# Kernel optimization log

Measured on AMD Instinct MI355X. Metric: run time of the kernel, lower is better.

## Reference

```python
import jax, jax.numpy as jnp
import numpy as np

OUT_F, IN_F = 4096, 4096
GROUP = 128
NGROUPS = IN_F // GROUP  # 32


def setup_inputs() -> dict:
    key = jax.random.key(0)
    k1, k2, k3, k4 = jax.random.split(key, 4)
    x = jax.random.normal(k1, (4, 2048, IN_F), dtype=jnp.float32)
    # 4-bit codes stored as integers in [0, 16)
    compressed_weight = jax.random.randint(k2, (OUT_F, IN_F), 0, 16, dtype=jnp.int32)
    scale = jax.random.uniform(k3, (OUT_F, NGROUPS), dtype=jnp.float32)
    offset = jax.random.normal(k4, (OUT_F, NGROUPS), dtype=jnp.float32)
    return {"x": x, "compressed_weight": compressed_weight, "scale": scale, "offset": offset}


def reference(x, compressed_weight, scale, offset):
    # group-wise dequant: w[o, g, j] = code * scale[o, g] - offset[o, g]
    codes = compressed_weight.astype(scale.dtype).reshape(OUT_F, NGROUPS, GROUP)
    w = (codes * scale[..., None] - offset[..., None]).reshape(OUT_F, IN_F)
    # F.linear: x @ w.T  -> [B, S, OUT_F]
    return jnp.einsum('bsi,oi->bso', x, w.astype(x.dtype))
```

## Files before the change

kernel.cpp:

```cpp
#include <hip/hip_runtime.h>
#include <stdint.h>

#define OUT_F 4096
#define IN_F  4096
#define NGROUPS 32
#define BK 64
#define NT (IN_F / BK)

typedef __attribute__((ext_vector_type(4))) float    f32x4;
typedef __attribute__((ext_vector_type(8))) short    bf16x8;
typedef __attribute__((ext_vector_type(4))) int      i32x4;
typedef __attribute__((ext_vector_type(4))) uint32_t u32x4;

__device__ __forceinline__ ushort f2bf(float f) {
  union { float f; uint32_t u; } v; v.f = f;
  uint32_t r = v.u + 0x7FFFu + ((v.u >> 16) & 1u);
  return (ushort)(r >> 16);
}

__global__ void cvt_x_kernel(const float* __restrict__ x, ushort* __restrict__ xb, int n8) {
  int i = blockIdx.x * blockDim.x + threadIdx.x;
  if (i >= n8) return;
  const f32x4* xp = (const f32x4*)x;
  f32x4 a = xp[2 * i], b = xp[2 * i + 1];
  u32x4 o;
  o.x = (uint32_t)f2bf(a.x) | ((uint32_t)f2bf(a.y) << 16);
  o.y = (uint32_t)f2bf(a.z) | ((uint32_t)f2bf(a.w) << 16);
  o.z = (uint32_t)f2bf(b.x) | ((uint32_t)f2bf(b.y) << 16);
  o.w = (uint32_t)f2bf(b.z) | ((uint32_t)f2bf(b.w) << 16);
  ((u32x4*)xb)[i] = o;
}

__global__ void dequant_w_kernel(const int* __restrict__ cw,
                                 const float* __restrict__ sc,
                                 const float* __restrict__ of,
                                 ushort* __restrict__ wb) {
  int t = blockIdx.x * blockDim.x + threadIdx.x;
  int o  = t >> 9;
  int k0 = (t & 511) << 3;
  int g  = k0 >> 7;
  float s   = sc[o * NGROUPS + g];
  float off = of[o * NGROUPS + g];
  const i32x4* cp = (const i32x4*)(cw + (size_t)o * IN_F + k0);
  i32x4 c0 = cp[0], c1 = cp[1];
  u32x4 out;
  out.x = (uint32_t)f2bf((float)c0.x * s - off) | ((uint32_t)f2bf((float)c0.y * s - off) << 16);
  out.y = (uint32_t)f2bf((float)c0.z * s - off) | ((uint32_t)f2bf((float)c0.w * s - off) << 16);
  out.z = (uint32_t)f2bf((float)c1.x * s - off) | ((uint32_t)f2bf((float)c1.y * s - off) << 16);
  out.w = (uint32_t)f2bf((float)c1.z * s - off) | ((uint32_t)f2bf((float)c1.w * s - off) << 16);
  *(u32x4*)(wb + (size_t)o * IN_F + k0) = out;
}


#define BAR() do { asm volatile("" ::: "memory"); __builtin_amdgcn_s_barrier(); asm volatile("" ::: "memory"); } while (0)

#define GLLDS(gp, lp) __builtin_amdgcn_global_load_lds( \
  (const __attribute__((address_space(1))) uint32_t*)(const void*)(gp), \
  (__attribute__((address_space(3))) uint32_t*)(void*)(lp), 16, 0, 0)

#define STAGE_A(buf, kt) do { \
  _Pragma("unroll") for (int h_ = 0; h_ < 2; ++h_) \
  _Pragma("unroll") for (int c_ = 0; c_ < 2; ++c_) \
    GLLDS(A + (size_t)(m0 + h_ * 128 + c_ * 64 + stRow) * IN_F + (kt) * BK + sl * 8, \
          ldsb + (buf) * 65536 + h_ * 16384 + c_ * 8192 + wid * 1024); \
} while (0)

#define STAGE_B_HALF(buf, kt, h_) do { \
  _Pragma("unroll") for (int c_ = 0; c_ < 2; ++c_) \
    GLLDS(B + (size_t)(n0 + (h_) * 128 + c_ * 64 + stRow) * IN_F + (kt) * BK + sl * 8, \
          ldsb + (buf) * 65536 + 32768 + (h_) * 16384 + c_ * 8192 + wid * 1024); \
} while (0)

#define RD_A(base, i0) do { \
  _Pragma("unroll") for (int i_ = 0; i_ < 4; ++i_) { \
    Ar[i_][0] = *(const bf16x8*)((base) + ((i0) + i_) * 2048 + off0); \
    Ar[i_][1] = *(const bf16x8*)((base) + ((i0) + i_) * 2048 + off1); \
  } } while (0)

#define RD_B(dst, j0) do { \
  _Pragma("unroll") for (int j_ = 0; j_ < 2; ++j_) { \
    dst[j_][0] = *(const bf16x8*)(bC + ((j0) + j_) * 2048 + off0); \
    dst[j_][1] = *(const bf16x8*)(bC + ((j0) + j_) * 2048 + off1); \
  } } while (0)

#define MFMAQ(I0, J0, Bset) do { \
  __builtin_amdgcn_s_setprio(1); \
  _Pragma("unroll") for (int i_ = 0; i_ < 4; ++i_) \
  _Pragma("unroll") for (int j_ = 0; j_ < 2; ++j_) { \
    acc[(I0) + i_][(J0) + j_] = __builtin_amdgcn_mfma_f32_16x16x32_bf16(Ar[i_][0], Bset[j_][0], acc[(I0) + i_][(J0) + j_], 0, 0, 0); \
    acc[(I0) + i_][(J0) + j_] = __builtin_amdgcn_mfma_f32_16x16x32_bf16(Ar[i_][1], Bset[j_][1], acc[(I0) + i_][(J0) + j_], 0, 0, 0); \
  } \
  __builtin_amdgcn_s_setprio(0); \
} while (0)

__global__ __launch_bounds__(512, 2) void gemm256(const ushort* __restrict__ A,
                                                  const ushort* __restrict__ B,
                                                  float* __restrict__ C, int M) {
  __shared__ ushort lds[65536];
  char* ldsb = (char*)lds;

  const int nmt = M >> 8;
  const int nwg = gridDim.x;
  int wg = blockIdx.x;
  if ((nwg & 7) == 0) wg = (wg & 7) * (nwg >> 3) + (wg >> 3);
  const int bn = wg / nmt;
  const int bm = wg % nmt;
  const int m0 = bm << 8, n0 = bn << 8;

  const int tid  = threadIdx.x;
  const int lane = tid & 63;
  const int wid  = tid >> 6;
  const int wr   = wid >> 2;
  const int wc   = wid & 3;

  const int stRow = wid * 8 + (lane >> 3);
  const int sl    = (lane & 7) ^ (lane >> 3);

  const int frow = lane & 15;
  const int g    = lane >> 4;
  const int off0 = frow * 128 + (((g    ) ^ (lane & 7)) << 4);
  const int off1 = frow * 128 + (((4 + g) ^ (lane & 7)) << 4);

  f32x4 acc[8][4] = {};
  bf16x8 Ar[4][2], Bl[2][2], Bh[2][2];

  STAGE_A(0, 0);
  STAGE_B_HALF(0, 0, 0);
  STAGE_B_HALF(0, 0, 1);
  STAGE_A(1, 1);
  asm volatile("s_waitcnt vmcnt(4)" ::: "memory");
  BAR();
  RD_A(ldsb + wr * 16384, 0);

#pragma unroll 1
  for (int t = 0; t < NT; ++t) {
    const int cur = t & 1, nxt = cur ^ 1;
    const char* aC = ldsb + cur * 65536 + wr * 16384;
    const char* aN = ldsb + nxt * 65536 + wr * 16384;
    const char* bC = ldsb + cur * 65536 + 32768 + (wc >> 1) * 16384 + (wc & 1) * 8192;

    RD_B(Bl, 0);
    RD_B(Bh, 2);
    if (t + 1 < NT) STAGE_B_HALF(nxt, t + 1, 0);
    BAR();
    MFMAQ(0, 0, Bl);

    if (t + 1 < NT) STAGE_B_HALF(nxt, t + 1, 1);
    BAR();
    MFMAQ(0, 2, Bh);
    RD_A(aC, 4);
    if (t + 1 < NT) { asm volatile("s_waitcnt vmcnt(4)" ::: "memory"); }
    BAR();

    MFMAQ(4, 2, Bh);
    BAR();

    if (t + 2 < NT) STAGE_A(cur, t + 2);
    MFMAQ(4, 0, Bl);
    if (t + 1 < NT) {
      RD_A(aN, 0);
      if (t + 2 < NT) { asm volatile("s_waitcnt vmcnt(4)" ::: "memory"); }
      else            { asm volatile("s_waitcnt vmcnt(0)" ::: "memory"); }
    }
    BAR();
  }

  const int crow0 = m0 + wr * 128 + (g << 2);
  const int ccol0 = n0 + wc * 64 + frow;
#pragma unroll
  for (int mf = 0; mf < 8; ++mf)
#pragma unroll
    for (int nf = 0; nf < 4; ++nf)
#pragma unroll
      for (int q = 0; q < 4; ++q)
        C[(size_t)(crow0 + mf * 16 + q) * OUT_F + (ccol0 + nf * 16)] = acc[mf][nf][q];
}

__global__ void naive_kernel(const float* __restrict__ x, const int* __restrict__ cw,
                             const float* __restrict__ sc, const float* __restrict__ of,
                             float* __restrict__ out, int M) {
  int idx = blockIdx.x * blockDim.x + threadIdx.x;
  if (idx >= M * OUT_F) return;
  int o = idx & (OUT_F - 1);
  int m = idx >> 12;
  const float* xr = x + (size_t)m * IN_F;
  const int*   wr = cw + (size_t)o * IN_F;
  float acc = 0.f;
  for (int gg = 0; gg < NGROUPS; ++gg) {
    float s = sc[o * NGROUPS + gg], off = of[o * NGROUPS + gg];
#pragma unroll 8
    for (int k = 0; k < 128; ++k) {
      int kk = (gg << 7) + k;
      acc += xr[kk] * ((float)wr[kk] * s - off);
    }
  }
  out[idx] = acc;
}

extern "C" void kernel_launch(void* const* d_in, const int* in_sizes, int n_in,
                              void* d_out, int out_size, void* d_ws, size_t ws_size,
                              hipStream_t stream) {
  const float* x  = (const float*)d_in[0];
  const int*   cw = (const int*)d_in[1];
  const float* sc = (const float*)d_in[2];
  const float* of = (const float*)d_in[3];
  float* out = (float*)d_out;
  const int M = in_sizes[0] / IN_F;

  const size_t xb_bytes = (size_t)M * IN_F * 2;
  const size_t wb_bytes = (size_t)OUT_F * IN_F * 2;

  if (ws_size >= xb_bytes + wb_bytes && (M % 256) == 0) {
    ushort* xb = (ushort*)d_ws;
    ushort* wb = (ushort*)((char*)d_ws + xb_bytes);

    int n8 = (M * IN_F) / 8;
    cvt_x_kernel<<<(n8 + 255) / 256, 256, 0, stream>>>(x, xb, n8);

    int nw8 = (OUT_F * IN_F) / 8;
    dequant_w_kernel<<<(nw8 + 255) / 256, 256, 0, stream>>>(cw, sc, of, wb);

    dim3 grid((M / 256) * (OUT_F / 256));
    gemm256<<<grid, 512, 0, stream>>>(xb, wb, out, M);
  } else {
    int total = M * OUT_F;
    naive_kernel<<<(total + 255) / 256, 256, 0, stream>>>(x, cw, sc, of, out, M);
  }
}
```

Baseline: 291.0 us.

## Switch GEMM to 32x32x16 MFMA with k-sliced double-buffered register pipeline

Replaces the 16x16x32 bf16 MFMA tiling with 32x32x16 MFMA instructions, so each wave computes 4x2 32x32 tiles per k-slice. The main loop is restructured to ping-pong register fragment sets across four k-slices, with A and B staged together for tile t+2 and one fewer barrier per iteration. The aim is fewer LDS reads per FLOP and better MFMA issue density. In exchange the vmcnt bookkeeping and epilogue store layout change, and the bigger accumulator fragments may raise register pressure.

```diff
diff --git a/kernel.cpp b/kernel.cpp
--- a/kernel.cpp
+++ b/kernel.cpp
@@ -7,10 +7,11 @@
 #define BK 64
 #define NT (IN_F / BK)
 
-typedef __attribute__((ext_vector_type(4))) float    f32x4;
-typedef __attribute__((ext_vector_type(8))) short    bf16x8;
-typedef __attribute__((ext_vector_type(4))) int      i32x4;
-typedef __attribute__((ext_vector_type(4))) uint32_t u32x4;
+typedef __attribute__((ext_vector_type(4)))  float    f32x4;
+typedef __attribute__((ext_vector_type(16))) float    f32x16;
+typedef __attribute__((ext_vector_type(8)))  short    bf16x8;
+typedef __attribute__((ext_vector_type(4)))  int      i32x4;
+typedef __attribute__((ext_vector_type(4)))  uint32_t u32x4;
 
 __device__ __forceinline__ ushort f2bf(float f) {
   union { float f; uint32_t u; } v; v.f = f;
@@ -59,37 +60,29 @@
   (__attribute__((address_space(3))) uint32_t*)(void*)(lp), 16, 0, 0)
 
 #define STAGE_A(buf, kt) do { \
-  _Pragma("unroll") for (int h_ = 0; h_ < 2; ++h_) \
-  _Pragma("unroll") for (int c_ = 0; c_ < 2; ++c_) \
-    GLLDS(A + (size_t)(m0 + h_ * 128 + c_ * 64 + stRow) * IN_F + (kt) * BK + sl * 8, \
-          ldsb + (buf) * 65536 + h_ * 16384 + c_ * 8192 + wid * 1024); \
-} while (0)
-
-#define STAGE_B_HALF(buf, kt, h_) do { \
-  _Pragma("unroll") for (int c_ = 0; c_ < 2; ++c_) \
-    GLLDS(B + (size_t)(n0 + (h_) * 128 + c_ * 64 + stRow) * IN_F + (kt) * BK + sl * 8, \
-          ldsb + (buf) * 65536 + 32768 + (h_) * 16384 + c_ * 8192 + wid * 1024); \
-} while (0)
-
-#define RD_A(base, i0) do { \
-  _Pragma("unroll") for (int i_ = 0; i_ < 4; ++i_) { \
-    Ar[i_][0] = *(const bf16x8*)((base) + ((i0) + i_) * 2048 + off0); \
-    Ar[i_][1] = *(const bf16x8*)((base) + ((i0) + i_) * 2048 + off1); \
-  } } while (0)
-
-#define RD_B(dst, j0) do { \
-  _Pragma("unroll") for (int j_ = 0; j_ < 2; ++j_) { \
-    dst[j_][0] = *(const bf16x8*)(bC + ((j0) + j_) * 2048 + off0); \
-    dst[j_][1] = *(const bf16x8*)(bC + ((j0) + j_) * 2048 + off1); \
-  } } while (0)
-
-#define MFMAQ(I0, J0, Bset) do { \
+  _Pragma("unroll") for (int q_ = 0; q_ < 4; ++q_) \
+    GLLDS(A + (size_t)(m0 + q_ * 64 + stRow) * IN_F + (kt) * BK + sl * 8, \
+          ldsb + (buf) * 65536 + q_ * 8192 + wid * 1024); \
+} while (0)
+
+#define STAGE_B(buf, kt) do { \
+  _Pragma("unroll") for (int q_ = 0; q_ < 4; ++q_) \
+    GLLDS(B + (size_t)(n0 + q_ * 64 + stRow) * IN_F + (kt) * BK + sl * 8, \
+          ldsb + (buf) * 65536 + 32768 + q_ * 8192 + wid * 1024); \
+} while (0)
+
+#define RD_SLICE(SET, S, aX, bX) do { \
+  _Pragma("unroll") for (int i_ = 0; i_ < 4; ++i_) \
+    A_[SET][i_] = *(const bf16x8*)((aX) + (i_ * 32 + lw) * 128 + kOff[S]); \
+  _Pragma("unroll") for (int j_ = 0; j_ < 2; ++j_) \
+    B_[SET][j_] = *(const bf16x8*)((bX) + (j_ * 32 + lw) * 128 + kOff[S]); \
+} while (0)
+
+#define MFMA_SLICE(SET) do { \
   __builtin_amdgcn_s_setprio(1); \
   _Pragma("unroll") for (int i_ = 0; i_ < 4; ++i_) \
-  _Pragma("unroll") for (int j_ = 0; j_ < 2; ++j_) { \
-    acc[(I0) + i_][(J0) + j_] = __builtin_amdgcn_mfma_f32_16x16x32_bf16(Ar[i_][0], Bset[j_][0], acc[(I0) + i_][(J0) + j_], 0, 0, 0); \
-    acc[(I0) + i_][(J0) + j_] = __builtin_amdgcn_mfma_f32_16x16x32_bf16(Ar[i_][1], Bset[j_][1], acc[(I0) + i_][(J0) + j_], 0, 0, 0); \
-  } \
+  _Pragma("unroll") for (int j_ = 0; j_ < 2; ++j_) \
+    acc[i_][j_] = __builtin_amdgcn_mfma_f32_32x32x16_bf16(A_[SET][i_], B_[SET][j_], acc[i_][j_], 0, 0, 0); \
   __builtin_amdgcn_s_setprio(0); \
 } while (0)
 
@@ -116,64 +109,56 @@
   const int stRow = wid * 8 + (lane >> 3);
   const int sl    = (lane & 7) ^ (lane >> 3);
 
-  const int frow = lane & 15;
-  const int g    = lane >> 4;
-  const int off0 = frow * 128 + (((g    ) ^ (lane & 7)) << 4);
-  const int off1 = frow * 128 + (((4 + g) ^ (lane & 7)) << 4);
-
-  f32x4 acc[8][4] = {};
-  bf16x8 Ar[4][2], Bl[2][2], Bh[2][2];
-
-  STAGE_A(0, 0);
-  STAGE_B_HALF(0, 0, 0);
-  STAGE_B_HALF(0, 0, 1);
-  STAGE_A(1, 1);
-  asm volatile("s_waitcnt vmcnt(4)" ::: "memory");
+  const int lw = lane & 31;
+  const int h  = lane >> 5;
+  int kOff[4];
+#pragma unroll
+  for (int s = 0; s < 4; ++s) kOff[s] = ((2 * s + h) ^ (lane & 7)) << 4;
+
+  f32x16 acc[4][2] = {};
+  bf16x8 A_[2][4], B_[2][2];
+
+  STAGE_A(0, 0); STAGE_B(0, 0);
+  STAGE_A(1, 1); STAGE_B(1, 1);
+  asm volatile("s_waitcnt vmcnt(8)" ::: "memory");
   BAR();
-  RD_A(ldsb + wr * 16384, 0);
+  RD_SLICE(0, 0, ldsb + wr * 16384, ldsb + 32768 + wc * 8192);
 
 #pragma unroll 1
   for (int t = 0; t < NT; ++t) {
     const int cur = t & 1, nxt = cur ^ 1;
     const char* aC = ldsb + cur * 65536 + wr * 16384;
+    const char* bC = ldsb + cur * 65536 + 32768 + wc * 8192;
     const char* aN = ldsb + nxt * 65536 + wr * 16384;
-    const char* bC = ldsb + cur * 65536 + 32768 + (wc >> 1) * 16384 + (wc & 1) * 8192;
-
-    RD_B(Bl, 0);
-    RD_B(Bh, 2);
-    if (t + 1 < NT) STAGE_B_HALF(nxt, t + 1, 0);
+    const char* bN = ldsb + nxt * 65536 + 32768 + wc * 8192;
+
+    RD_SLICE(1, 1, aC, bC);
+    MFMA_SLICE(0);
+    RD_SLICE(0, 2, aC, bC);
+    MFMA_SLICE(1);
     BAR();
-    MFMAQ(0, 0, Bl);
-
-    if (t + 1 < NT) STAGE_B_HALF(nxt, t + 1, 1);
+
+    RD_SLICE(1, 3, aC, bC);
+    if (t + 2 < NT) { STAGE_A(cur, t + 2); STAGE_B(cur, t + 2); }
+    MFMA_SLICE(0);
+    if (t + 2 < NT)      { asm volatile("s_waitcnt vmcnt(8)" ::: "memory"); }
+    else if (t + 1 < NT) { asm volatile("s_waitcnt vmcnt(0)" ::: "memory"); }
     BAR();
-    MFMAQ(0, 2, Bh);
-    RD_A(aC, 4);
-    if (t + 1 < NT) { asm volatile("s_waitcnt vmcnt(4)" ::: "memory"); }
-    BAR();
-
-    MFMAQ(4, 2, Bh);
-    BAR();
-
-    if (t + 2 < NT) STAGE_A(cur, t + 2);
-    MFMAQ(4, 0, Bl);
-    if (t + 1 < NT) {
-      RD_A(aN, 0);
-      if (t + 2 < NT) { asm volatile("s_waitcnt vmcnt(4)" ::: "memory"); }
-      else            { asm volatile("s_waitcnt vmcnt(0)" ::: "memory"); }
-    }
-    BAR();
+    if (t + 1 < NT) RD_SLICE(0, 0, aN, bN);
+    MFMA_SLICE(1);
   }
 
-  const int crow0 = m0 + wr * 128 + (g << 2);
-  const int ccol0 = n0 + wc * 64 + frow;
-#pragma unroll
-  for (int mf = 0; mf < 8; ++mf)
-#pragma unroll
-    for (int nf = 0; nf < 4; ++nf)
-#pragma unroll
-      for (int q = 0; q < 4; ++q)
-        C[(size_t)(crow0 + mf * 16 + q) * OUT_F + (ccol0 + nf * 16)] = acc[mf][nf][q];
+  const int crow = m0 + wr * 128;
+  const int ccol = n0 + wc * 64 + lw;
+#pragma unroll
+  for (int i = 0; i < 4; ++i)
+#pragma unroll
+    for (int j = 0; j < 2; ++j)
+#pragma unroll
+      for (int p = 0; p < 4; ++p)
+#pragma unroll
+        for (int q = 0; q < 4; ++q)
+          C[(size_t)(crow + i * 32 + 8 * p + 4 * h + q) * OUT_F + (ccol + j * 32)] = acc[i][j][4 * p + q];
 }
 
 __global__ void naive_kernel(const float* __restrict__ x, const int* __restrict__ cw,
```

New measurement: 313.6 us. +7.8%, slower.
